# Kernel optimization log

Hardware: AMD Instinct MI355X
Metric: run time of the kernel (lower is better)

Reference implementation:

```python
import jax, jax.numpy as jnp
import numpy as np


def setup_inputs() -> dict:
    key = jax.random.key(0)
    k1, k2, k3 = jax.random.split(key, 3)
    B, V, C = 2, 20000, 9
    KS, OUT, NB = 9, 16, 16
    x = jax.random.normal(k1, (B, V, C), dtype=jnp.float32)
    # Glorot-normal-ish init for W [coord, kernel_size, out]
    W = jax.random.normal(k2, (C, KS, OUT), dtype=jnp.float32) * np.sqrt(2.0 / (C + KS * OUT)).astype(np.float32)
    # adj indexes a zero-padded vertex table of size V+1; 0 means 'no neighbor'
    adj = jax.random.randint(k3, (V, NB), 0, V + 1, dtype=jnp.int32)
    return {"x": x, "W": W, "adj": adj}


def reference(x, W, adj):
    B, V, C = x.shape
    _, KS, OUT = W.shape  # note: code only runs when C == KS (source bug, see notes)
    NB = adj.shape[1]
    # degree normalization: 1/count_nonzero(adj) per vertex, 0 if no neighbors
    deg = jnp.sum(adj != 0, axis=-1).astype(x.dtype)  # [V]
    inv_deg = jnp.where(deg > 0, 1.0 / jnp.where(deg > 0, deg, 1.0), 0.0)  # [V]
    # wx = x @ reshape(W, [C, KS*OUT])
    wx = jnp.einsum('bvc,cf->bvf', x, W.reshape(C, KS * OUT))  # [B,V,KS*OUT]
    zero_pad = jnp.zeros((B, 1, KS * OUT), dtype=x.dtype)
    patches = jnp.concatenate([zero_pad, wx], axis=1)[:, adj]  # [B,V,NB,KS*OUT]
    patches = patches.reshape(B, V, NB, KS, OUT)
    # pseudo-coordinate diffs on padded raw input
    pad_x = jnp.concatenate([jnp.zeros((B, 1, C), dtype=x.dtype), x], axis=1)
    nbx = pad_x[:, adj]  # [B,V,NB,C]
    mask = (adj != 0)[None, :, :, None]
    diff = jnp.where(mask, x[:, :, None, :] - nbx, jnp.zeros_like(nbx))  # [B,V,NB,C]
    # source bug: matmul with u is discarded; softmax over coord axis
    q = jax.nn.softmax(diff, axis=-1)  # [B,V,NB,C] with C == KS
    # weighted aggregation over neighbors, then degree norm, then sum over kernels
    agg = jnp.einsum('bvnk,bvnko->bvko', q, patches)  # [B,V,KS,OUT]
    agg = agg * inv_deg[None, :, None, None]
    out = jnp.sum(agg, axis=2)  # [B,V,OUT]
    return jax.nn.relu(out)
```

## Files before the change

### kernel.cpp

```cpp
#include <hip/hip_runtime.h>
#include <math.h>

#define Bb   2
#define Vv   20000
#define Cc   9
#define KS   9
#define OUTn 16
#define NB   16

__global__ __launch_bounds__(256) void nlayer_kernel(
    const float* __restrict__ x,
    const float* __restrict__ W,
    const int*   __restrict__ adj,
    float* __restrict__ out)
{
    __shared__ float sW[Cc * KS * OUTn];
    for (int i = threadIdx.x; i < Cc * KS * OUTn; i += 256) sW[i] = W[i];
    __syncthreads();

    int tid = blockIdx.x * 256 + threadIdx.x;
    if (tid >= Bb * Vv) return;
    int b = tid / Vv;
    int v = tid - b * Vv;

    int a[NB];
    #pragma unroll
    for (int n = 0; n < NB; ++n) a[n] = adj[v * NB + n];

    int deg = 0;
    #pragma unroll
    for (int n = 0; n < NB; ++n) deg += (a[n] != 0);

    const float* xb = x + (size_t)b * Vv * Cc;

    float xv[Cc];
    #pragma unroll
    for (int c = 0; c < Cc; ++c) xv[c] = xb[(size_t)v * Cc + c];

    float s[KS][Cc];
    #pragma unroll
    for (int k = 0; k < KS; ++k)
        #pragma unroll
        for (int c = 0; c < Cc; ++c) s[k][c] = 0.0f;

    for (int n = 0; n < NB; ++n) {
        int j = a[n];
        if (j == 0) continue;
        const float* xp = xb + (size_t)(j - 1) * Cc;
        float xn[Cc];
        #pragma unroll
        for (int c = 0; c < Cc; ++c) xn[c] = xp[c];

        float d[Cc];
        float m = -INFINITY;
        #pragma unroll
        for (int c = 0; c < Cc; ++c) { d[c] = xv[c] - xn[c]; m = fmaxf(m, d[c]); }
        float e[Cc];
        float sum = 0.0f;
        #pragma unroll
        for (int c = 0; c < Cc; ++c) { e[c] = __expf(d[c] - m); sum += e[c]; }
        float inv = 1.0f / sum;

        #pragma unroll
        for (int k = 0; k < KS; ++k) {
            float qk = e[k] * inv;
            #pragma unroll
            for (int c = 0; c < Cc; ++c) s[k][c] = fmaf(qk, xn[c], s[k][c]);
        }
    }

    float invdeg = (deg > 0) ? (1.0f / (float)deg) : 0.0f;

    float acc[OUTn];
    #pragma unroll
    for (int o = 0; o < OUTn; ++o) acc[o] = 0.0f;

    #pragma unroll
    for (int c = 0; c < Cc; ++c) {
        #pragma unroll
        for (int k = 0; k < KS; ++k) {
            float sv = s[k][c];
            const float* wp = &sW[(c * KS + k) * OUTn];
            #pragma unroll
            for (int o = 0; o < OUTn; ++o) acc[o] = fmaf(sv, wp[o], acc[o]);
        }
    }

    float* op = out + (size_t)tid * OUTn;
    #pragma unroll
    for (int o = 0; o < OUTn; ++o) {
        float r = acc[o] * invdeg;
        op[o] = (r > 0.0f) ? r : 0.0f;
    }
}

extern "C" void kernel_launch(void* const* d_in, const int* in_sizes, int n_in,
                              void* d_out, int out_size, void* d_ws, size_t ws_size,
                              hipStream_t stream) {
    const float* x   = (const float*)d_in[0];
    const float* W   = (const float*)d_in[1];
    const int*   adj = (const int*)d_in[2];
    float*       out = (float*)d_out;

    const int total = Bb * Vv;
    const int block = 256;
    const int grid  = (total + block - 1) / block;
    nlayer_kernel<<<grid, block, 0, stream>>>(x, W, adj, out);
}
```

Before: 72.72 us.

## Split each vertex across four lanes with shuffle reduction and vectorized IO

Each vertex is now handled by four threads. Each thread processes four neighbors with branchless masking and software-pipelined row loads. The 81 partial sums and the degree are then combined with quad xor-shuffles, and each lane computes and stores four of the sixteen outputs using float4 loads of adjacency, W and the output. This raises parallelism from 40k threads to 160k and spreads the gather latency across lanes. In exchange it adds 162 shuffles per thread and does redundant softmax work for missing neighbors.

```diff
diff --git a/kernel.cpp b/kernel.cpp
--- a/kernel.cpp
+++ b/kernel.cpp
@@ -7,6 +7,44 @@
 #define KS   9
 #define OUTn 16
 #define NB   16
+#define LPV  4
+
+static_assert(NB % LPV == 0, "neighbors must split evenly across lanes");
+static_assert(OUTn % LPV == 0, "outputs must split evenly across lanes");
+static_assert((Bb * Vv * LPV) % 256 == 0, "grid must exactly cover work");
+
+__device__ __forceinline__ float quad_sum(float x) {
+    x += __shfl_xor(x, 1, 64);
+    x += __shfl_xor(x, 2, 64);
+    return x;
+}
+
+__device__ __forceinline__ void loadrow(float (&dst)[Cc],
+                                        const float* __restrict__ xb, int j) {
+    const float* p = xb + (j > 0 ? j - 1 : 0) * Cc;
+    #pragma unroll
+    for (int c = 0; c < Cc; ++c) dst[c] = p[c];
+}
+
+__device__ __forceinline__ void accum(const float (&xv)[Cc],
+                                      const float (&xn)[Cc],
+                                      float mskf,
+                                      float (&s)[KS][Cc]) {
+    float d[Cc];
+    float m = -INFINITY;
+    #pragma unroll
+    for (int c = 0; c < Cc; ++c) { d[c] = xv[c] - xn[c]; m = fmaxf(m, d[c]); }
+    float sum = 0.0f;
+    #pragma unroll
+    for (int c = 0; c < Cc; ++c) { d[c] = __expf(d[c] - m); sum += d[c]; }
+    float invs = mskf / sum;
+    #pragma unroll
+    for (int k = 0; k < KS; ++k) {
+        float qk = d[k] * invs;
+        #pragma unroll
+        for (int c = 0; c < Cc; ++c) s[k][c] = fmaf(qk, xn[c], s[k][c]);
+    }
+}
 
 __global__ __launch_bounds__(256) void nlayer_kernel(
     const float* __restrict__ x,
@@ -14,28 +52,30 @@
     const int*   __restrict__ adj,
     float* __restrict__ out)
 {
-    __shared__ float sW[Cc * KS * OUTn];
-    for (int i = threadIdx.x; i < Cc * KS * OUTn; i += 256) sW[i] = W[i];
+    __shared__ float4 sW[(Cc * KS * OUTn) / 4];
+    {
+        const float4* Wv = (const float4*)W;
+        int t = threadIdx.x;
+        if (t < (Cc * KS * OUTn) / 4) sW[t] = Wv[t];
+        t += 256;
+        if (t < (Cc * KS * OUTn) / 4) sW[t] = Wv[t];
+    }
     __syncthreads();
 
-    int tid = blockIdx.x * 256 + threadIdx.x;
-    if (tid >= Bb * Vv) return;
-    int b = tid / Vv;
-    int v = tid - b * Vv;
+    const int tid  = blockIdx.x * 256 + threadIdx.x;
+    const int vert = tid >> 2;
+    if (vert >= Bb * Vv) return;
+    const int sl   = tid & 3;
+    const int b    = vert / Vv;
+    const int v    = vert - b * Vv;
 
-    int a[NB];
-    #pragma unroll
-    for (int n = 0; n < NB; ++n) a[n] = adj[v * NB + n];
+    const int4 aj = ((const int4*)adj)[v * (NB / 4) + sl];
 
-    int deg = 0;
-    #pragma unroll
-    for (int n = 0; n < NB; ++n) deg += (a[n] != 0);
-
-    const float* xb = x + (size_t)b * Vv * Cc;
+    const float* xb = x + b * (Vv * Cc);
 
     float xv[Cc];
     #pragma unroll
-    for (int c = 0; c < Cc; ++c) xv[c] = xb[(size_t)v * Cc + c];
+    for (int c = 0; c < Cc; ++c) xv[c] = xb[v * Cc + c];
 
     float s[KS][Cc];
     #pragma unroll
@@ -43,55 +83,49 @@
         #pragma unroll
         for (int c = 0; c < Cc; ++c) s[k][c] = 0.0f;
 
-    for (int n = 0; n < NB; ++n) {
-        int j = a[n];
-        if (j == 0) continue;
-        const float* xp = xb + (size_t)(j - 1) * Cc;
-        float xn[Cc];
+    const float m0 = (aj.x != 0) ? 1.0f : 0.0f;
+    const float m1 = (aj.y != 0) ? 1.0f : 0.0f;
+    const float m2 = (aj.z != 0) ? 1.0f : 0.0f;
+    const float m3 = (aj.w != 0) ? 1.0f : 0.0f;
+
+    float xnA[Cc], xnB[Cc];
+    loadrow(xnA, xb, aj.x);
+    loadrow(xnB, xb, aj.y);
+    accum(xv, xnA, m0, s);
+    loadrow(xnA, xb, aj.z);
+    accum(xv, xnB, m1, s);
+    loadrow(xnB, xb, aj.w);
+    accum(xv, xnA, m2, s);
+    accum(xv, xnB, m3, s);
+
+    float degf = quad_sum(m0 + m1 + m2 + m3);
+    #pragma unroll
+    for (int k = 0; k < KS; ++k)
         #pragma unroll
-        for (int c = 0; c < Cc; ++c) xn[c] = xp[c];
+        for (int c = 0; c < Cc; ++c) s[k][c] = quad_sum(s[k][c]);
 
-        float d[Cc];
-        float m = -INFINITY;
-        #pragma unroll
-        for (int c = 0; c < Cc; ++c) { d[c] = xv[c] - xn[c]; m = fmaxf(m, d[c]); }
-        float e[Cc];
-        float sum = 0.0f;
-        #pragma unroll
-        for (int c = 0; c < Cc; ++c) { e[c] = __expf(d[c] - m); sum += e[c]; }
-        float inv = 1.0f / sum;
+    const float invdeg = (degf > 0.0f) ? (1.0f / degf) : 0.0f;
 
-        #pragma unroll
-        for (int k = 0; k < KS; ++k) {
-            float qk = e[k] * inv;
-            #pragma unroll
-            for (int c = 0; c < Cc; ++c) s[k][c] = fmaf(qk, xn[c], s[k][c]);
-        }
-    }
-
-    float invdeg = (deg > 0) ? (1.0f / (float)deg) : 0.0f;
-
-    float acc[OUTn];
-    #pragma unroll
-    for (int o = 0; o < OUTn; ++o) acc[o] = 0.0f;
-
+    float4 acc = make_float4(0.f, 0.f, 0.f, 0.f);
     #pragma unroll
     for (int c = 0; c < Cc; ++c) {
         #pragma unroll
         for (int k = 0; k < KS; ++k) {
-            float sv = s[k][c];
-            const float* wp = &sW[(c * KS + k) * OUTn];
-            #pragma unroll
-            for (int o = 0; o < OUTn; ++o) acc[o] = fmaf(sv, wp[o], acc[o]);
+            const float  sv = s[k][c];
+            const float4 w4 = sW[(c * KS + k) * (OUTn / 4) + sl];
+            acc.x = fmaf(sv, w4.x, acc.x);
+            acc.y = fmaf(sv, w4.y, acc.y);
+            acc.z = fmaf(sv, w4.z, acc.z);
+            acc.w = fmaf(sv, w4.w, acc.w);
         }
     }
 
-    float* op = out + (size_t)tid * OUTn;
-    #pragma unroll
-    for (int o = 0; o < OUTn; ++o) {
-        float r = acc[o] * invdeg;
-        op[o] = (r > 0.0f) ? r : 0.0f;
-    }
+    float4 r;
+    r.x = fmaxf(acc.x * invdeg, 0.0f);
+    r.y = fmaxf(acc.y * invdeg, 0.0f);
+    r.z = fmaxf(acc.z * invdeg, 0.0f);
+    r.w = fmaxf(acc.w * invdeg, 0.0f);
+    ((float4*)out)[vert * (OUTn / 4) + sl] = r;
 }
 
 extern "C" void kernel_launch(void* const* d_in, const int* in_sizes, int n_in,
@@ -102,8 +136,8 @@
     const int*   adj = (const int*)d_in[2];
     float*       out = (float*)d_out;
 
-    const int total = Bb * Vv;
+    const int total = Bb * Vv * LPV;
     const int block = 256;
-    const int grid  = (total + block - 1) / block;
+    const int grid  = total / block;
     nlayer_kernel<<<grid, block, 0, stream>>>(x, W, adj, out);
 }
```

After: 72.19 us. No clear change (-0.7%).
